# Kernel optimization log

Hardware: AMD Instinct MI355X
Metric: run time of the kernel (lower is better)

Reference implementation:

```python
import jax, jax.numpy as jnp
import numpy as np

NEG_INF = 1e20  # matches INF in the torch source
EPS = 1e-12     # F.normalize default eps
THRESHOLD = 0.1  # config.graph_learn_epsilon_label2label


def setup_inputs() -> dict:
    key = jax.random.key(0)
    k1, k2, k3, k4, k5 = jax.random.split(key, 5)
    L, E, E_PT, H = 2048, 512, 300, 16
    return {
        "label_embedding": jax.random.normal(k1, (L, E), dtype=jnp.float32),
        "pretrained_label_embedding": jax.random.normal(k2, (L, E_PT), dtype=jnp.float32),
        "W_pt": jax.random.normal(k3, (H, E_PT), dtype=jnp.float32) * 0.1,
        "W_gcn0": jax.random.normal(k4, (E, E), dtype=jnp.float32) * (1.0 / np.sqrt(E)),
        "W_gcn1": jax.random.normal(k5, (E, E), dtype=jnp.float32) * (1.0 / np.sqrt(E)),
    }


def _weighted_cosine(input_pt, W_pt):
    # W_pt: [H, E_pt]; input_pt: [L, E_pt]
    w2 = W_pt ** 2                                  # [H, E_pt]
    h = input_pt[None, :, :] * w2[:, None, :]       # [H, L, E_pt]
    norm = jnp.linalg.norm(h, axis=-1, keepdims=True)
    h_norm = h / jnp.maximum(norm, EPS)             # F.normalize(p=2, dim=-1)
    # mean over heads of per-head cosine similarity: [L, L]
    scores = jnp.einsum("hle,hme->hlm", h_norm, h_norm).mean(axis=0)
    return scores


def reference(label_embedding, pretrained_label_embedding, W_pt, W_gcn0, W_gcn1):
    # 1) metric-based graph structure learning
    scores_cosine = _weighted_cosine(pretrained_label_embedding, W_pt)
    scores = jnp.where(scores_cosine >= THRESHOLD, scores_cosine, -NEG_INF)
    adj = jax.nn.softmax(scores, axis=-1)           # [L, L]

    # 2) 2-layer GCN message passing (bias=None, batch_norm=False, eval-mode dropout)
    x = jax.nn.relu(adj @ (label_embedding @ W_gcn0))
    x = jax.nn.relu(adj @ (x @ W_gcn1))
    return x
```

## Files before the change

kernel.cpp:

```cpp
#include <hip/hip_runtime.h>
#include <hip/hip_bf16.h>


typedef __attribute__((ext_vector_type(8))) short bf16x8;
typedef __attribute__((ext_vector_type(4))) float f32x4;

#define L_DIM 2048
#define EPT 300
#define H_DIM 16
#define KDIM 4800
#define WINDOW 5.5e-4f

__global__ void compute_y_kernel(const float* __restrict__ xpt,
                                 const float* __restrict__ Wpt,
                                 __hip_bfloat16* __restrict__ Y,
                                 float* __restrict__ norms) {
  int gw = (blockIdx.x * 256 + threadIdx.x) >> 6;
  int lane = threadIdx.x & 63;
  int i = gw >> 4, h = gw & 15;
  const float* x = xpt + i * EPT;
  const float* w = Wpt + h * EPT;
  float v[5];
  float ss = 0.f;
#pragma unroll
  for (int t = 0; t < 5; ++t) {
    int e = lane + 64 * t;
    float val = 0.f;
    if (e < EPT) {
      float we = w[e];
      val = x[e] * we * we;
    }
    v[t] = val;
    ss += val * val;
  }
#pragma unroll
  for (int o = 32; o >= 1; o >>= 1) ss += __shfl_xor(ss, o, 64);
  float n = fmaxf(sqrtf(ss), 1e-12f);
  if (lane == 0) norms[i * H_DIM + h] = n;
  float scale = 0.25f / n;
#pragma unroll
  for (int t = 0; t < 5; ++t) {
    int e = lane + 64 * t;
    if (e < EPT) Y[(size_t)i * KDIM + h * EPT + e] = __float2bfloat16(v[t] * scale);
  }
}

template <int BM, int BN, bool RELU, bool OUT_BF16, bool MIRROR, bool SPLITX>
__global__ __launch_bounds__(256) void gemm_bt(const __hip_bfloat16* __restrict__ A,
                                               const __hip_bfloat16* __restrict__ B,
                                               void* __restrict__ C0v, void* __restrict__ C1v,
                                               int M, int N, int K) {
  constexpr int WMG = BM / 64;
  constexpr int WNG = 4 / WMG;
  constexpr int NC = BN / (16 * WNG);
  int bx = blockIdx.x;
  int kbeg = 0, kend = K;
  if (SPLITX) {
    const int xhalf = gridDim.x >> 1;
    const int khalf = ((K >> 1) + 63) & ~63;
    if (bx >= xhalf) {
      bx -= xhalf;
      kbeg = khalf;
    } else {
      kend = khalf;
    }
  }
  const int row0 = blockIdx.y * BM, col0 = bx * BN;
  if (MIRROR && col0 + BN <= row0) return;
  const bool do_mirror = MIRROR && (col0 > row0);
  __shared__ __attribute__((aligned(16))) __hip_bfloat16 As[2][BM * 64];
  __shared__ __attribute__((aligned(16))) __hip_bfloat16 Bs[2][BN * 64];
  const int tid = threadIdx.x;
  const int lane = tid & 63;
  const int wave = tid >> 6;
  const int wm = wave / WNG, wn = wave % WNG;
  const int r = lane & 15, q = lane >> 4;
  const int srow = tid >> 3;
  const int schunk = (tid & 7) ^ (srow & 7);

  f32x4 acc[4][NC];
#pragma unroll
  for (int a = 0; a < 4; ++a)
#pragma unroll
    for (int b = 0; b < NC; ++b) {
      f32x4 z = {0.f, 0.f, 0.f, 0.f};
      acc[a][b] = z;
    }

  const int niter = (kend - kbeg) >> 6;

#define STAGE(bufi, k0)                                                                       \
  {                                                                                           \
    _Pragma("unroll") for (int it = 0; it < BM / 32; ++it) {                                  \
      __builtin_amdgcn_global_load_lds(                                                       \
          (const __attribute__((address_space(1))) void*)(A + (size_t)(row0 + it * 32 + srow) * K + \
                                                          (k0) + schunk * 8),                 \
          (__attribute__((address_space(3))) void*)(&As[bufi][(it * 256 + tid) * 8]), 16, 0, 0); \
    }                                                                                         \
    _Pragma("unroll") for (int it = 0; it < BN / 32; ++it) {                                  \
      __builtin_amdgcn_global_load_lds(                                                       \
          (const __attribute__((address_space(1))) void*)(B + (size_t)(col0 + it * 32 + srow) * K + \
                                                          (k0) + schunk * 8),                 \
          (__attribute__((address_space(3))) void*)(&Bs[bufi][(it * 256 + tid) * 8]), 16, 0, 0); \
    }                                                                                         \
  }

  STAGE(0, kbeg)
  for (int k = 0; k < niter; ++k) {
    __syncthreads();
    if (k + 1 < niter) STAGE((k + 1) & 1, kbeg + ((k + 1) << 6))
    const __hip_bfloat16* as = As[k & 1];
    const __hip_bfloat16* bs = Bs[k & 1];
#pragma unroll
    for (int kk = 0; kk < 2; ++kk) {
      const int ch = ((kk * 4 + q) ^ (r & 7)) * 8;
      bf16x8 af[4], bfr[NC];
#pragma unroll
      for (int t = 0; t < 4; ++t)
        af[t] = *(const bf16x8*)(as + (wm * 64 + t * 16 + r) * 64 + ch);
#pragma unroll
      for (int c = 0; c < NC; ++c)
        bfr[c] = *(const bf16x8*)(bs + (wn * 16 * NC + c * 16 + r) * 64 + ch);
#pragma unroll
      for (int tm = 0; tm < 4; ++tm)
#pragma unroll
        for (int tn = 0; tn < NC; ++tn)
          acc[tm][tn] = __builtin_amdgcn_mfma_f32_16x16x32_bf16(af[tm], bfr[tn], acc[tm][tn], 0, 0, 0);
    }
  }
#undef STAGE
  float* dst = (float*)(SPLITX ? (kbeg > 0 ? C1v : C0v) : C0v);
#pragma unroll
  for (int tm = 0; tm < 4; ++tm) {
    int gr0 = row0 + wm * 64 + tm * 16 + q * 4;
#pragma unroll
    for (int tn = 0; tn < NC; ++tn) {
      int gc = col0 + wn * 16 * NC + tn * 16 + r;
#pragma unroll
      for (int p = 0; p < 4; ++p) {
        float vv = acc[tm][tn][p];
        if (RELU) vv = fmaxf(vv, 0.f);
        if (OUT_BF16) {
          ((__hip_bfloat16*)C0v)[(size_t)(gr0 + p) * N + gc] = __float2bfloat16(vv);
        } else {
          dst[(size_t)(gr0 + p) * N + gc] = vv;
          if (do_mirror) dst[(size_t)gc * N + (gr0 + p)] = vv;
        }
      }
    }
  }
}

__global__ __launch_bounds__(256) void scan_repair(float* __restrict__ S,
                                                   const float* __restrict__ xpt,
                                                   const float* __restrict__ Wpt,
                                                   const float* __restrict__ norms) {
  __shared__ int lqueue[2048];
  __shared__ int lcount;
  if (threadIdx.x == 0) lcount = 0;
  __syncthreads();
  const int row = blockIdx.x;
  const int base_idx = row * 2048;
#pragma unroll
  for (int t = 0; t < 2; ++t) {
    int col = t * 1024 + threadIdx.x * 4;
    if (col + 4 <= row) continue;
    float4 v = *(const float4*)(S + base_idx + col);
    float vv[4] = {v.x, v.y, v.z, v.w};
#pragma unroll
    for (int u = 0; u < 4; ++u) {
      int j = col + u;
      if (j >= row && fabsf(vv[u] - 0.1f) < WINDOW) {
        int p = atomicAdd(&lcount, 1);
        lqueue[p] = j;
      }
    }
  }
  __syncthreads();
  const int n = lcount;
  if (n == 0) return;
  const int lane = threadIdx.x & 63;
  const int wave = threadIdx.x >> 6;
  const int i = row;
  float xiv[5];
  {
    const float* xi = xpt + i * EPT;
#pragma unroll
    for (int t = 0; t < 5; ++t) {
      int idx = lane + 64 * t;
      xiv[t] = idx < EPT ? xi[idx] : 0.f;
    }
  }
  for (int k = wave; k < n; k += 4) {
    int j = lqueue[k];
    const float* xj = xpt + j * EPT;
    float pre[5];
#pragma unroll
    for (int t = 0; t < 5; ++t) {
      int idx = lane + 64 * t;
      pre[t] = idx < EPT ? xiv[t] * xj[idx] : 0.f;
    }
    float accv = 0.f;
#pragma unroll
    for (int h = 0; h < H_DIM; ++h) {
      float ph = 0.f;
#pragma unroll
      for (int t = 0; t < 5; ++t) {
        int idx = lane + 64 * t;
        if (idx < EPT) {
          float w = Wpt[h * EPT + idx];
          float w2 = w * w;
          ph += pre[t] * (w2 * w2);
        }
      }
      accv += ph * (1.f / (norms[i * H_DIM + h] * norms[j * H_DIM + h]));
    }
#pragma unroll
    for (int o = 32; o >= 1; o >>= 1) accv += __shfl_xor(accv, o, 64);
    if (lane == 0) {
      float val = accv * (1.f / 16.f);
      S[(size_t)i * L_DIM + j] = val;
      S[(size_t)j * L_DIM + i] = val;
    }
  }
}

__global__ __launch_bounds__(256) void post_kernel(const float* __restrict__ S,
                                                   __hip_bfloat16* __restrict__ adj,
                                                   const float* __restrict__ label,
                                                   __hip_bfloat16* __restrict__ Lbf,
                                                   const float* __restrict__ W0,
                                                   const float* __restrict__ W1,
                                                   __hip_bfloat16* __restrict__ W0t,
                                                   __hip_bfloat16* __restrict__ W1t) {
  __shared__ float red[4];
  __shared__ float tile[32][33];
  const int b = blockIdx.x;
  const int tid = threadIdx.x;
  if (b < 2048) {
    const int row = b;
    const float* s = S + (size_t)row * L_DIM;
    float m = -1e30f;
    for (int j = tid; j < L_DIM; j += 256) {
      float v = s[j];
      if (v >= 0.1f && v > m) m = v;
    }
#pragma unroll
    for (int o = 32; o >= 1; o >>= 1) m = fmaxf(m, __shfl_xor(m, o, 64));
    if ((tid & 63) == 0) red[tid >> 6] = m;
    __syncthreads();
    m = fmaxf(fmaxf(red[0], red[1]), fmaxf(red[2], red[3]));
    float sum = 0.f;
    for (int j = tid; j < L_DIM; j += 256) {
      float v = s[j];
      if (v >= 0.1f) sum += __expf(v - m);
    }
#pragma unroll
    for (int o = 32; o >= 1; o >>= 1) sum += __shfl_xor(sum, o, 64);
    __syncthreads();
    if ((tid & 63) == 0) red[tid >> 6] = sum;
    __syncthreads();
    sum = red[0] + red[1] + red[2] + red[3];
    float inv = 1.f / sum;
    for (int j = tid; j < L_DIM; j += 256) {
      float v = s[j];
      float a = (v >= 0.1f) ? __expf(v - m) * inv : 0.f;
      adj[(size_t)row * L_DIM + j] = __float2bfloat16(a);
    }
    return;
  }
  if (b < 6144) {
    int i = (b - 2048) * 256 + tid;
    Lbf[i] = __float2bfloat16(label[i]);
    return;
  }
  int local = b - 6144;
  const bool first = local < 256;
  const float* src = first ? W0 : W1;
  __hip_bfloat16* dst = first ? W0t : W1t;
  int rem = local & 255;
  int c0 = (rem & 15) * 32, r0 = (rem >> 4) * 32;
  int tx = tid & 31, ty = tid >> 5;
  for (int i2 = ty; i2 < 32; i2 += 8) tile[i2][tx] = src[(size_t)(r0 + i2) * 512 + c0 + tx];
  __syncthreads();
  for (int i2 = ty; i2 < 32; i2 += 8)
    dst[(size_t)(c0 + i2) * 512 + r0 + tx] = __float2bfloat16(tile[tx][i2]);
}

__global__ void combine_relu_bf16(const float* __restrict__ P0, const float* __restrict__ P1,
                                  __hip_bfloat16* __restrict__ X) {
  int i = blockIdx.x * 256 + threadIdx.x;
  float4 a = ((const float4*)P0)[i];
  float4 b = ((const float4*)P1)[i];
  __hip_bfloat16 o0 = __float2bfloat16(fmaxf(a.x + b.x, 0.f));
  __hip_bfloat16 o1 = __float2bfloat16(fmaxf(a.y + b.y, 0.f));
  __hip_bfloat16 o2 = __float2bfloat16(fmaxf(a.z + b.z, 0.f));
  __hip_bfloat16 o3 = __float2bfloat16(fmaxf(a.w + b.w, 0.f));
  X[4 * i + 0] = o0;
  X[4 * i + 1] = o1;
  X[4 * i + 2] = o2;
  X[4 * i + 3] = o3;
}

__global__ void combine_relu_f32(const float* __restrict__ P0, const float* __restrict__ P1,
                                 float* __restrict__ X) {
  int i = blockIdx.x * 256 + threadIdx.x;
  float4 a = ((const float4*)P0)[i];
  float4 b = ((const float4*)P1)[i];
  float4 v;
  v.x = fmaxf(a.x + b.x, 0.f);
  v.y = fmaxf(a.y + b.y, 0.f);
  v.z = fmaxf(a.z + b.z, 0.f);
  v.w = fmaxf(a.w + b.w, 0.f);
  ((float4*)X)[i] = v;
}

extern "C" void kernel_launch(void* const* d_in, const int* in_sizes, int n_in, void* d_out,
                              int out_size, void* d_ws, size_t ws_size, hipStream_t stream) {
  const float* label = (const float*)d_in[0];
  const float* xpt = (const float*)d_in[1];
  const float* Wpt = (const float*)d_in[2];
  const float* W0 = (const float*)d_in[3];
  const float* W1 = (const float*)d_in[4];
  float* out = (float*)d_out;

  char* ws = (char*)d_ws;
  __hip_bfloat16* Y = (__hip_bfloat16*)ws;
  float* S = (float*)(ws + 19660800);
  float* norms = (float*)(ws + 36438016);
  float* P0 = (float*)(ws + 36569088);
  float* P1 = (float*)(ws + 40763392);
  __hip_bfloat16* adj = (__hip_bfloat16*)ws;
  __hip_bfloat16* Lbf = (__hip_bfloat16*)(ws + 8388608);
  __hip_bfloat16* W0t = (__hip_bfloat16*)(ws + 10485760);
  __hip_bfloat16* W1t = (__hip_bfloat16*)(ws + 11010048);
  __hip_bfloat16* T0t = (__hip_bfloat16*)(ws + 11534336);
  __hip_bfloat16* X1 = (__hip_bfloat16*)(ws + 13631488);
  __hip_bfloat16* T1t = (__hip_bfloat16*)(ws + 15728640);

  compute_y_kernel<<<8192, 256, 0, stream>>>(xpt, Wpt, Y, norms);
  gemm_bt<64, 64, false, false, true, false><<<dim3(32, 32), 256, 0, stream>>>(Y, Y, S, nullptr, 2048, 2048, KDIM);
  scan_repair<<<2048, 256, 0, stream>>>(S, xpt, Wpt, norms);
  post_kernel<<<6656, 256, 0, stream>>>(S, adj, label, Lbf, W0, W1, W0t, W1t);
  gemm_bt<64, 64, false, true, false, false><<<dim3(32, 8), 256, 0, stream>>>(W0t, Lbf, T0t, nullptr, 512, 2048, 512);
  gemm_bt<64, 64, false, false, false, true><<<dim3(16, 32), 256, 0, stream>>>(adj, T0t, P0, P1, 2048, 512, 2048);
  combine_relu_bf16<<<1024, 256, 0, stream>>>(P0, P1, X1);
  gemm_bt<64, 64, false, true, false, false><<<dim3(32, 8), 256, 0, stream>>>(W1t, X1, T1t, nullptr, 512, 2048, 512);
  gemm_bt<64, 64, false, false, false, true><<<dim3(16, 32), 256, 0, stream>>>(adj, T1t, P0, P1, 2048, 512, 2048);
  combine_relu_f32<<<1024, 256, 0, stream>>>(P0, P1, out);
}
```

Measured before the change: 205.1 us.

## Compute cosine Gram matrix with int8 MFMA and widen repair window

Quantizes the normalized weighted embeddings to int8 instead of bf16 and computes the L×L score matrix with a new int8 MFMA Gram kernel. The kernel skips lower-triangle tiles and mirrors the results, and stages tiles with direct global-to-LDS loads. The threshold repair scan now recomputes every entry above a lower cutoff rather than a narrow window around the threshold, with a queue bound added. This halves Gram-matrix operand bytes and uses higher-throughput int8 MFMA. In exchange, coarser quantization pushes more entries into the exact fp32 repair path, which may cost time in scan_repair.

```diff
diff --git a/kernel.cpp b/kernel.cpp
--- a/kernel.cpp
+++ b/kernel.cpp
@@ -4,16 +4,18 @@
 
 typedef __attribute__((ext_vector_type(8))) short bf16x8;
 typedef __attribute__((ext_vector_type(4))) float f32x4;
+typedef __attribute__((ext_vector_type(4))) int i32x4;
 
 #define L_DIM 2048
 #define EPT 300
 #define H_DIM 16
 #define KDIM 4800
-#define WINDOW 5.5e-4f
+#define SCAN_LO 0.0985f
+#define QSCALE 508.0f
 
 __global__ void compute_y_kernel(const float* __restrict__ xpt,
                                  const float* __restrict__ Wpt,
-                                 __hip_bfloat16* __restrict__ Y,
+                                 signed char* __restrict__ Y,
                                  float* __restrict__ norms) {
   int gw = (blockIdx.x * 256 + threadIdx.x) >> 6;
   int lane = threadIdx.x & 63;
@@ -41,7 +43,76 @@
 #pragma unroll
   for (int t = 0; t < 5; ++t) {
     int e = lane + 64 * t;
-    if (e < EPT) Y[(size_t)i * KDIM + h * EPT + e] = __float2bfloat16(v[t] * scale);
+    if (e < EPT) {
+      int qv = __float2int_rn(v[t] * scale * QSCALE);
+      Y[(size_t)i * KDIM + h * EPT + e] = (signed char)qv;
+    }
+  }
+}
+
+__global__ __launch_bounds__(256) void gram_i8(const signed char* __restrict__ Y,
+                                               float* __restrict__ S) {
+  const int id = blockIdx.x;
+  const int bx = (id & 7) | (((id >> 3) & 3) << 3);
+  const int by = id >> 5;
+  const int row0 = by * 64, col0 = bx * 64;
+  if (col0 + 64 <= row0) return;
+  const bool do_mirror = (col0 > row0);
+  __shared__ __attribute__((aligned(16))) signed char As[2][4096];
+  __shared__ __attribute__((aligned(16))) signed char Bs[2][4096];
+  const int tid = threadIdx.x;
+  const int lane = tid & 63;
+  const int wn = tid >> 6;
+  const int r = lane & 15, q = lane >> 4;
+  const int srow = tid >> 2;
+  const int sc = (tid & 3) ^ ((srow >> 2) & 3);
+
+  i32x4 acc[4];
+#pragma unroll
+  for (int t = 0; t < 4; ++t) {
+    i32x4 z = {0, 0, 0, 0};
+    acc[t] = z;
+  }
+  const int niter = KDIM / 64;
+
+#define STAGEI(bufi, k0)                                                                       \
+  {                                                                                            \
+    __builtin_amdgcn_global_load_lds(                                                          \
+        (const __attribute__((address_space(1))) void*)(Y + (size_t)(row0 + srow) * KDIM +     \
+                                                        (k0) + sc * 16),                       \
+        (__attribute__((address_space(3))) void*)(&As[bufi][tid * 16]), 16, 0, 0);             \
+    __builtin_amdgcn_global_load_lds(                                                          \
+        (const __attribute__((address_space(1))) void*)(Y + (size_t)(col0 + srow) * KDIM +     \
+                                                        (k0) + sc * 16),                       \
+        (__attribute__((address_space(3))) void*)(&Bs[bufi][tid * 16]), 16, 0, 0);             \
+  }
+
+  STAGEI(0, 0)
+  for (int k = 0; k < niter; ++k) {
+    __syncthreads();
+    if (k + 1 < niter) STAGEI((k + 1) & 1, (k + 1) * 64)
+    const signed char* as = As[k & 1];
+    const signed char* bs = Bs[k & 1];
+    const int ch = (q ^ ((r >> 2) & 3)) * 16;
+    i32x4 bfrag = *(const i32x4*)(bs + (wn * 16 + r) * 64 + ch);
+#pragma unroll
+    for (int t = 0; t < 4; ++t) {
+      i32x4 afrag = *(const i32x4*)(as + (t * 16 + r) * 64 + ch);
+      acc[t] = __builtin_amdgcn_mfma_i32_16x16x64_i8(afrag, bfrag, acc[t], 0, 0, 0);
+    }
+  }
+#undef STAGEI
+  const float dq = 1.0f / (QSCALE * QSCALE);
+#pragma unroll
+  for (int t = 0; t < 4; ++t) {
+    int gr0 = row0 + t * 16 + q * 4;
+    int gc = col0 + wn * 16 + r;
+#pragma unroll
+    for (int p = 0; p < 4; ++p) {
+      float vv = (float)acc[t][p] * dq;
+      S[(size_t)(gr0 + p) * L_DIM + gc] = vv;
+      if (do_mirror) S[(size_t)gc * L_DIM + (gr0 + p)] = vv;
+    }
   }
 }
 
@@ -170,14 +241,14 @@
 #pragma unroll
     for (int u = 0; u < 4; ++u) {
       int j = col + u;
-      if (j >= row && fabsf(vv[u] - 0.1f) < WINDOW) {
+      if (j >= row && vv[u] > SCAN_LO) {
         int p = atomicAdd(&lcount, 1);
-        lqueue[p] = j;
+        if (p < 2048) lqueue[p] = j;
       }
     }
   }
   __syncthreads();
-  const int n = lcount;
+  const int n = min(lcount, 2048);
   if (n == 0) return;
   const int lane = threadIdx.x & 63;
   const int wave = threadIdx.x >> 6;
@@ -325,7 +396,7 @@
   float* out = (float*)d_out;
 
   char* ws = (char*)d_ws;
-  __hip_bfloat16* Y = (__hip_bfloat16*)ws;
+  signed char* Y = (signed char*)ws;
   float* S = (float*)(ws + 19660800);
   float* norms = (float*)(ws + 36438016);
   float* P0 = (float*)(ws + 36569088);
@@ -339,7 +410,7 @@
   __hip_bfloat16* T1t = (__hip_bfloat16*)(ws + 15728640);
 
   compute_y_kernel<<<8192, 256, 0, stream>>>(xpt, Wpt, Y, norms);
-  gemm_bt<64, 64, false, false, true, false><<<dim3(32, 32), 256, 0, stream>>>(Y, Y, S, nullptr, 2048, 2048, KDIM);
+  gram_i8<<<1024, 256, 0, stream>>>(Y, S);
   scan_repair<<<2048, 256, 0, stream>>>(S, xpt, Wpt, norms);
   post_kernel<<<6656, 256, 0, stream>>>(S, adj, label, Lbf, W0, W1, W0t, W1t);
   gemm_bt<64, 64, false, true, false, false><<<dim3(32, 8), 256, 0, stream>>>(W0t, Lbf, T0t, nullptr, 512, 2048, 512);
```

After: 352.5 us. 1.72x slower.
